# Kernel optimization log

Hardware: AMD Instinct MI355X
Metric: run time of the kernel (lower is better)

The kernel has to match this reference:

```python
import jax, jax.numpy as jnp
import numpy as np

B, M, A, F = 8, 512, 16, 128  # batch, atoms/messages, irrep dim (n_ang_mom**2=16), feature channels
CG_DENSITY = 0.25             # CG coefficient tensors are highly sparse; emulate with a random mask


def setup_inputs() -> dict:
    key = jax.random.key(0)
    kx, ky, kc, km = jax.random.split(key, 4)
    x = jax.random.normal(kx, (B, M, A, F), dtype=jnp.float32)
    y = jax.random.normal(ky, (B, M, A, F), dtype=jnp.float32)
    # stand-in for cgc_multiplier(n_ang_mom): sparse [a, d, c] Clebsch-Gordan coefficient tensor
    cgc_dense = jax.random.normal(kc, (A, A, A), dtype=jnp.float32)
    mask = jax.random.bernoulli(km, CG_DENSITY, (A, A, A))
    cgc = jnp.where(mask, cgc_dense, 0.0)
    return {"x": x, "y": y, "cgc": cgc}


def reference(x, y, cgc):
    # TensorProductContractionLayer.call: triple contraction over irrep indices a, c
    # x: [b,m,a,f], y: [b,m,c,f], cgc: [a,d,c] -> res: [b,m,d,f]
    return jnp.einsum('bmaf,bmcf,adc->bmdf', x, y, cgc)
```

## Files before the change

kernel.cpp:

```cpp
#include <hip/hip_runtime.h>
#include <hip/hip_bf16.h>


typedef __attribute__((ext_vector_type(8))) short  short8;
typedef __attribute__((ext_vector_type(4))) float  floatx4;
typedef __attribute__((ext_vector_type(4))) unsigned int uintx4;

#define AA 16
#define FF 128

static __device__ __forceinline__ unsigned int pack_bf16_2(float lo, float hi) {
    __hip_bfloat162 h = __float22bfloat162_rn(make_float2(lo, hi));
    unsigned int u;
    __builtin_memcpy(&u, &h, 4);
    return u;
}

__global__ __launch_bounds__(256, 4)
void tpc_mfma_kernel(const float* __restrict__ x,
                     const float* __restrict__ y,
                     const float* __restrict__ cgc,
                     float* __restrict__ out) {
    const int wave = threadIdx.x >> 6;
    const int lane = threadIdx.x & 63;
    const int L    = lane & 15;
    const int quad = lane >> 4;
    const int qh   = quad >> 1;
    const int c0   = (quad & 1) * 8;

    const int bm = blockIdx.x * 4 + wave;

    short8 wfrag[8];
#pragma unroll
    for (int t = 0; t < 8; ++t) {
        const float* wp = cgc + (2 * t + qh) * (AA * AA) + L * AA + c0;
        const floatx4 w0 = *(const floatx4*)(wp);
        const floatx4 w1 = *(const floatx4*)(wp + 4);
        uintx4 u;
        u.x = pack_bf16_2(w0.x, w0.y);
        u.y = pack_bf16_2(w0.z, w0.w);
        u.z = pack_bf16_2(w1.x, w1.y);
        u.w = pack_bf16_2(w1.z, w1.w);
        wfrag[t] = __builtin_bit_cast(short8, u);
    }

    const float* xb = x   + (size_t)bm * (AA * FF);
    const float* yb = y   + (size_t)bm * (AA * FF);
    float*       ob = out + (size_t)bm * (AA * FF);

#pragma unroll 1
    for (int tile = 0; tile < 8; ++tile) {
        const int f = tile * 16 + L;

        float yv[8], xv[8];
#pragma unroll
        for (int j = 0; j < 8; ++j) yv[j] = yb[(c0 + j) * FF + f];
#pragma unroll
        for (int t = 0; t < 8; ++t) xv[t] = xb[(2 * t + qh) * FF + f];

        floatx4 acc = {0.f, 0.f, 0.f, 0.f};
#pragma unroll
        for (int t = 0; t < 8; ++t) {
            const float xs = xv[t];
            uintx4 u;
            u.x = pack_bf16_2(xs * yv[0], xs * yv[1]);
            u.y = pack_bf16_2(xs * yv[2], xs * yv[3]);
            u.z = pack_bf16_2(xs * yv[4], xs * yv[5]);
            u.w = pack_bf16_2(xs * yv[6], xs * yv[7]);
            const short8 bfrag = __builtin_bit_cast(short8, u);
            acc = __builtin_amdgcn_mfma_f32_16x16x32_bf16(wfrag[t], bfrag, acc, 0, 0, 0);
        }

#pragma unroll
        for (int r = 0; r < 4; ++r)
            ob[(quad * 4 + r) * FF + f] = acc[r];
    }
}

extern "C" void kernel_launch(void* const* d_in, const int* in_sizes, int n_in,
                              void* d_out, int out_size, void* d_ws, size_t ws_size,
                              hipStream_t stream) {
    const float* x   = (const float*)d_in[0];
    const float* y   = (const float*)d_in[1];
    const float* cgc = (const float*)d_in[2];
    float* out = (float*)d_out;

    hipLaunchKernelGGL(tpc_mfma_kernel, dim3(1024), dim3(256), 0, stream,
                       x, y, cgc, out);
}
```

Measured before the change: 115.0 us.

## Stage x/y tiles through LDS via direct global-to-LDS loads, one block per row

Each block now handles a single (b,m) slice. Its 256 threads cooperatively copy the whole 16x128 x and y tiles into shared memory with 16-byte global_load_lds transfers, replacing the per-wave strided scalar global loads. Each wave then reads its operands from LDS and processes two 16-wide feature tiles with two independent MFMA accumulator chains, instead of looping over eight tiles. The aim is wider, coalesced global traffic, four times as many blocks for latency hiding, and more instruction-level parallelism. The cost is 16 KB of LDS per block plus a barrier, which may limit occupancy.

```diff
diff --git a/kernel.cpp b/kernel.cpp
--- a/kernel.cpp
+++ b/kernel.cpp
@@ -16,19 +16,41 @@
     return u;
 }
 
+static __device__ __forceinline__ void gload_lds16(const float* g, float* l) {
+    __builtin_amdgcn_global_load_lds(
+        (const __attribute__((address_space(1))) void*)g,
+        (__attribute__((address_space(3))) void*)l,
+        16, 0, 0);
+}
+
 __global__ __launch_bounds__(256, 4)
-void tpc_mfma_kernel(const float* __restrict__ x,
-                     const float* __restrict__ y,
-                     const float* __restrict__ cgc,
-                     float* __restrict__ out) {
-    const int wave = threadIdx.x >> 6;
-    const int lane = threadIdx.x & 63;
+void tpc_mfma_lds_kernel(const float* __restrict__ x,
+                         const float* __restrict__ y,
+                         const float* __restrict__ cgc,
+                         float* __restrict__ out) {
+    __shared__ float lx[AA * FF];
+    __shared__ float ly[AA * FF];
+
+    const int tid  = threadIdx.x;
+    const int w    = tid >> 6;
+    const int lane = tid & 63;
     const int L    = lane & 15;
     const int quad = lane >> 4;
     const int qh   = quad >> 1;
     const int c0   = (quad & 1) * 8;
 
-    const int bm = blockIdx.x * 4 + wave;
+    const int bm = blockIdx.x;
+    const float* xb = x   + (size_t)bm * (AA * FF);
+    const float* yb = y   + (size_t)bm * (AA * FF);
+    float*       ob = out + (size_t)bm * (AA * FF);
+
+    {
+        const int off = w * 512 + lane * 4;
+        gload_lds16(xb + off,       lx + off);
+        gload_lds16(xb + off + 256, lx + off + 256);
+        gload_lds16(yb + off,       ly + off);
+        gload_lds16(yb + off + 256, ly + off + 256);
+    }
 
     short8 wfrag[8];
 #pragma unroll
@@ -44,36 +66,49 @@
         wfrag[t] = __builtin_bit_cast(short8, u);
     }
 
-    const float* xb = x   + (size_t)bm * (AA * FF);
-    const float* yb = y   + (size_t)bm * (AA * FF);
-    float*       ob = out + (size_t)bm * (AA * FF);
+    __syncthreads();
 
-#pragma unroll 1
-    for (int tile = 0; tile < 8; ++tile) {
-        const int f = tile * 16 + L;
+    const int f0 = w * 32 + L;
 
-        float yv[8], xv[8];
+    float xvA[8], xvB[8], yvA[8], yvB[8];
 #pragma unroll
-        for (int j = 0; j < 8; ++j) yv[j] = yb[(c0 + j) * FF + f];
+    for (int j = 0; j < 8; ++j) {
+        yvA[j] = ly[(c0 + j) * FF + f0];
+        yvB[j] = ly[(c0 + j) * FF + f0 + 16];
+    }
 #pragma unroll
-        for (int t = 0; t < 8; ++t) xv[t] = xb[(2 * t + qh) * FF + f];
+    for (int t = 0; t < 8; ++t) {
+        xvA[t] = lx[(2 * t + qh) * FF + f0];
+        xvB[t] = lx[(2 * t + qh) * FF + f0 + 16];
+    }
 
-        floatx4 acc = {0.f, 0.f, 0.f, 0.f};
+    floatx4 acc0 = {0.f, 0.f, 0.f, 0.f};
+    floatx4 acc1 = {0.f, 0.f, 0.f, 0.f};
 #pragma unroll
-        for (int t = 0; t < 8; ++t) {
-            const float xs = xv[t];
-            uintx4 u;
-            u.x = pack_bf16_2(xs * yv[0], xs * yv[1]);
-            u.y = pack_bf16_2(xs * yv[2], xs * yv[3]);
-            u.z = pack_bf16_2(xs * yv[4], xs * yv[5]);
-            u.w = pack_bf16_2(xs * yv[6], xs * yv[7]);
-            const short8 bfrag = __builtin_bit_cast(short8, u);
-            acc = __builtin_amdgcn_mfma_f32_16x16x32_bf16(wfrag[t], bfrag, acc, 0, 0, 0);
-        }
+    for (int t = 0; t < 8; ++t) {
+        uintx4 u;
+        float xs = xvA[t];
+        u.x = pack_bf16_2(xs * yvA[0], xs * yvA[1]);
+        u.y = pack_bf16_2(xs * yvA[2], xs * yvA[3]);
+        u.z = pack_bf16_2(xs * yvA[4], xs * yvA[5]);
+        u.w = pack_bf16_2(xs * yvA[6], xs * yvA[7]);
+        acc0 = __builtin_amdgcn_mfma_f32_16x16x32_bf16(
+                   wfrag[t], __builtin_bit_cast(short8, u), acc0, 0, 0, 0);
+
+        xs = xvB[t];
+        u.x = pack_bf16_2(xs * yvB[0], xs * yvB[1]);
+        u.y = pack_bf16_2(xs * yvB[2], xs * yvB[3]);
+        u.z = pack_bf16_2(xs * yvB[4], xs * yvB[5]);
+        u.w = pack_bf16_2(xs * yvB[6], xs * yvB[7]);
+        acc1 = __builtin_amdgcn_mfma_f32_16x16x32_bf16(
+                   wfrag[t], __builtin_bit_cast(short8, u), acc1, 0, 0, 0);
+    }
 
 #pragma unroll
-        for (int r = 0; r < 4; ++r)
-            ob[(quad * 4 + r) * FF + f] = acc[r];
+    for (int r = 0; r < 4; ++r) {
+        const int row = (quad * 4 + r) * FF;
+        ob[row + f0]      = acc0[r];
+        ob[row + f0 + 16] = acc1[r];
     }
 }
 
@@ -85,6 +120,6 @@
     const float* cgc = (const float*)d_in[2];
     float* out = (float*)d_out;
 
-    hipLaunchKernelGGL(tpc_mfma_kernel, dim3(1024), dim3(256), 0, stream,
+    hipLaunchKernelGGL(tpc_mfma_lds_kernel, dim3(4096), dim3(256), 0, stream,
                        x, y, cgc, out);
 }
```

Result: faster. 107.9 us (-6.2%).
